# Performance work log

Hardware: AMD Instinct MI355X
Metric: run time of the kernel (lower is better)

The kernel has to match this reference:

```python
import jax, jax.numpy as jnp
import numpy as np

B, T, D = 64, 1024, 512
U = 512  # num_units == input dim (GRULayer default)


def setup_inputs() -> dict:
    key = jax.random.key(0)
    k1, k2, k3, k4 = jax.random.split(key, 4)
    scale_k = 1.0 / np.sqrt(D)
    scale_r = 1.0 / np.sqrt(U)
    x = jax.random.normal(k1, (B, T, D), dtype=jnp.float32)
    kernel = jax.random.normal(k2, (D, 3 * U), dtype=jnp.float32) * scale_k
    recurrent_kernel = jax.random.normal(k3, (U, 3 * U), dtype=jnp.float32) * scale_r
    # Keras GRUCell reset_after=True: bias shape (2, 3U): input bias + recurrent bias
    bias = jax.random.normal(k4, (2, 3 * U), dtype=jnp.float32) * 0.01
    return {"x": x, "kernel": kernel, "recurrent_kernel": recurrent_kernel, "bias": bias}


def reference(x, kernel, recurrent_kernel, bias):
    """Keras GRUCell (reset_after=True) recurrence via layers.RNN.

    Returns only the final hidden state [B, U] (return_sequences=False).
    """
    b_i = bias[0]  # input bias [3U]
    b_r = bias[1]  # recurrent bias [3U]

    def step(h, x_t):
        # x_t: [B, D], h: [B, U]
        xm = x_t @ kernel + b_i                # [B, 3U]
        hm = h @ recurrent_kernel + b_r        # [B, 3U]
        xz, xr, xh = jnp.split(xm, 3, axis=-1)
        hz, hr, hh = jnp.split(hm, 3, axis=-1)
        z = jax.nn.sigmoid(xz + hz)            # update gate
        r = jax.nn.sigmoid(xr + hr)            # reset gate
        h_cand = jnp.tanh(xh + r * hh)
        h_new = z * h + (1.0 - z) * h_cand
        return h_new, None

    h0 = jnp.zeros((x.shape[0], U), dtype=x.dtype)
    xs = jnp.swapaxes(x, 0, 1)  # [T, B, D] for scan over time
    h_final, _ = jax.lax.scan(step, h0, xs)
    return h_final  # [B, U]
```

## Files before the change

kernel.cpp:

```cpp
#include <hip/hip_runtime.h>
#include <hip/hip_bf16.h>


typedef __attribute__((ext_vector_type(8))) short short8;
typedef __attribute__((ext_vector_type(4))) float f32x4;
typedef __attribute__((ext_vector_type(4))) unsigned int u32x4;

__device__ __forceinline__ unsigned short f2bf(float f) {
  unsigned u = __float_as_uint(f);
  u += 0x7FFFu + ((u >> 16) & 1u);
  return (unsigned short)(u >> 16);
}
__device__ __forceinline__ float bf2f(unsigned short s) {
  return __uint_as_float(((unsigned)s) << 16);
}

__global__ void transpose_cast(const float* __restrict__ src,
                               unsigned short* __restrict__ dst,
                               int R, int C) {
  __shared__ float tile[32][33];
  int c0 = blockIdx.x * 32, r0 = blockIdx.y * 32;
  int tx = threadIdx.x, ty = threadIdx.y;
#pragma unroll
  for (int i = 0; i < 4; i++) {
    tile[ty + i * 8][tx] = src[(size_t)(r0 + ty + i * 8) * C + c0 + tx];
  }
  __syncthreads();
#pragma unroll
  for (int i = 0; i < 4; i++) {
    dst[(size_t)(c0 + ty + i * 8) * R + r0 + tx] = f2bf(tile[tx][ty + i * 8]);
  }
}

__global__ __launch_bounds__(256) void xm_gemm(const float* __restrict__ x,
                                               const unsigned short* __restrict__ Wt,
                                               const float* __restrict__ bias,
                                               unsigned short* __restrict__ XM) {
  __shared__ unsigned short As[128][72];
  __shared__ unsigned short Bs[128][72];
  const int tid = threadIdx.x;
  const int bm = blockIdx.x;
  const int bn = blockIdx.y;
  const int wave = tid >> 6, lane = tid & 63;
  const int moff = (wave & 1) * 64, noff = (wave >> 1) * 64;

  f32x4 acc[4][4];
#pragma unroll
  for (int mt = 0; mt < 4; mt++)
#pragma unroll
    for (int nt = 0; nt < 4; nt++) acc[mt][nt] = (f32x4){0.f, 0.f, 0.f, 0.f};

  const int r = tid >> 1;
  const int kb = (tid & 1) * 32;
  const int rg = bm * 128 + r;
  const int bb = rg & 63, tt = rg >> 6;

  for (int k0 = 0; k0 < 512; k0 += 64) {
    const f32x4* xp4 = (const f32x4*)(x + ((size_t)bb * 1024 + tt) * 512 + k0 + kb);
#pragma unroll
    for (int j = 0; j < 4; j++) {
      f32x4 lo = xp4[2 * j];
      f32x4 hi = xp4[2 * j + 1];
      union { unsigned short us[8]; short8 v; } u;
      u.us[0] = f2bf(lo[0]); u.us[1] = f2bf(lo[1]); u.us[2] = f2bf(lo[2]); u.us[3] = f2bf(lo[3]);
      u.us[4] = f2bf(hi[0]); u.us[5] = f2bf(hi[1]); u.us[6] = f2bf(hi[2]); u.us[7] = f2bf(hi[3]);
      *(short8*)&As[r][kb + j * 8] = u.v;
    }
    const short8* wp8 = (const short8*)(Wt + (size_t)(bn * 128 + r) * 512 + k0 + kb);
#pragma unroll
    for (int j = 0; j < 4; j++) *(short8*)&Bs[r][kb + j * 8] = wp8[j];
    __syncthreads();

#pragma unroll
    for (int kk = 0; kk < 2; kk++) {
      short8 a[4], b[4];
#pragma unroll
      for (int mt = 0; mt < 4; mt++)
        a[mt] = *(const short8*)&As[moff + mt * 16 + (lane & 15)][kk * 32 + (lane >> 4) * 8];
#pragma unroll
      for (int nt = 0; nt < 4; nt++)
        b[nt] = *(const short8*)&Bs[noff + nt * 16 + (lane & 15)][kk * 32 + (lane >> 4) * 8];
#pragma unroll
      for (int mt = 0; mt < 4; mt++)
#pragma unroll
        for (int nt = 0; nt < 4; nt++)
          acc[mt][nt] = __builtin_amdgcn_mfma_f32_16x16x32_bf16(a[mt], b[nt], acc[mt][nt], 0, 0, 0);
    }
    __syncthreads();
  }

#pragma unroll
  for (int nt = 0; nt < 4; nt++) {
    const int cg = bn * 128 + noff + nt * 16 + (lane & 15);
    const float bi = bias[cg];
#pragma unroll
    for (int mt = 0; mt < 4; mt++) {
      const int rg2 = bm * 128 + moff + mt * 16 + (lane >> 4) * 4;
#pragma unroll
      for (int i = 0; i < 4; i++)
        XM[(size_t)(rg2 + i) * 1536 + cg] = f2bf(acc[mt][nt][i] + bi);
    }
  }
}

__global__ __launch_bounds__(256, 1) void gru_rec(const unsigned short* __restrict__ Rt,
                                                  const unsigned short* __restrict__ XM,
                                                  const float* __restrict__ bias,
                                                  unsigned int* ring,
                                                  unsigned int* flags,
                                                  float* __restrict__ out) {
  const int tid = threadIdx.x;
  const int lane = tid & 63;
  const int w = tid >> 6;
  const int blk = blockIdx.x;
  const int gi = blk >> 3;
  const int j = blk & 7;
  const int u0 = j * 64 + w * 16;
  const int col = lane & 15;
  const int krow = lane >> 4;
  const int hrow = col & 7;

  unsigned int* ring_g = ring + (size_t)gi * 4096;
  unsigned long long* ring64_g = (unsigned long long*)ring_g;
  unsigned int* flg = flags + gi * 32;

  __shared__ alignas(16) unsigned short hlds[8][512];

  short8 Bf[3][16];
#pragma unroll
  for (int g3 = 0; g3 < 3; g3++)
#pragma unroll
    for (int ks = 0; ks < 16; ks++)
      Bf[g3][ks] = *(const short8*)(Rt + (size_t)(g3 * 512 + u0 + col) * 512 + ks * 32 + krow * 8);

  const float br0 = bias[1536 + 0 * 512 + u0 + col];
  const float br1 = bias[1536 + 1 * 512 + u0 + col];
  const float br2 = bias[1536 + 2 * 512 + u0 + col];

  float hreg[4] = {0.f, 0.f, 0.f, 0.f};

  const int g1 = tid, g2 = tid + 256;
  const int r1 = g1 >> 6, c1s = (g1 & 63) ^ r1;
  const int r2 = g2 >> 6, c2s = (g2 & 63) ^ r2;

  unsigned short xc[3][4], xn[3][4];
#pragma unroll
  for (int g3 = 0; g3 < 3; g3++)
#pragma unroll
    for (int i = 0; i < 4; i++) {
      int batch = gi * 8 + ((krow * 4 + i) & 7);
      xc[g3][i] = XM[(size_t)batch * 1536 + g3 * 512 + u0 + col];
    }

#pragma unroll 1
  for (int t = 0; t < 1024; ++t) {
    f32x4 acc0 = (f32x4){0.f, 0.f, 0.f, 0.f};
    f32x4 acc1 = acc0, acc2 = acc0;

    if (t > 0) {
      if (w == 0) {
        const unsigned tgt = (unsigned)t;
        for (;;) {
          unsigned v = (lane < 8)
              ? __hip_atomic_load(&flg[lane], __ATOMIC_RELAXED, __HIP_MEMORY_SCOPE_AGENT)
              : tgt;
          if (__all((int)(v >= tgt))) break;
          __builtin_amdgcn_s_sleep(1);
        }
      }
      __syncthreads();

      const unsigned long long* rp = ring64_g + (size_t)((t + 1) & 1) * 1024;
      unsigned long long qa0 = __hip_atomic_load(rp + 2 * g1, __ATOMIC_RELAXED,
                                                 __HIP_MEMORY_SCOPE_AGENT);
      unsigned long long qa1 = __hip_atomic_load(rp + 2 * g1 + 1, __ATOMIC_RELAXED,
                                                 __HIP_MEMORY_SCOPE_AGENT);
      unsigned long long qb0 = __hip_atomic_load(rp + 2 * g2, __ATOMIC_RELAXED,
                                                 __HIP_MEMORY_SCOPE_AGENT);
      unsigned long long qb1 = __hip_atomic_load(rp + 2 * g2 + 1, __ATOMIC_RELAXED,
                                                 __HIP_MEMORY_SCOPE_AGENT);

      *(u32x4*)&hlds[r1][c1s * 8] =
          (u32x4){(unsigned)qa0, (unsigned)(qa0 >> 32), (unsigned)qa1, (unsigned)(qa1 >> 32)};
      *(u32x4*)&hlds[r2][c2s * 8] =
          (u32x4){(unsigned)qb0, (unsigned)(qb0 >> 32), (unsigned)qb1, (unsigned)(qb1 >> 32)};
      __syncthreads();

      short8 Af[16];
#pragma unroll
      for (int ks = 0; ks < 16; ++ks)
        Af[ks] = *(const short8*)&hlds[hrow][(((ks << 2) + krow) ^ hrow) * 8];
#pragma unroll
      for (int ks = 0; ks < 16; ++ks) {
        acc0 = __builtin_amdgcn_mfma_f32_16x16x32_bf16(Af[ks], Bf[0][ks], acc0, 0, 0, 0);
        acc1 = __builtin_amdgcn_mfma_f32_16x16x32_bf16(Af[ks], Bf[1][ks], acc1, 0, 0, 0);
        acc2 = __builtin_amdgcn_mfma_f32_16x16x32_bf16(Af[ks], Bf[2][ks], acc2, 0, 0, 0);
      }
    }

#pragma unroll
    for (int i = 0; i < 4; i++) {
      float hz = acc0[i] + br0;
      float hr = acc1[i] + br1;
      float hh = acc2[i] + br2;
      float xz = bf2f(xc[0][i]);
      float xr = bf2f(xc[1][i]);
      float xh = bf2f(xc[2][i]);
      float z = 1.f / (1.f + __expf(-(xz + hz)));
      float r = 1.f / (1.f + __expf(-(xr + hr)));
      float y = xh + r * hh;
      float ay = fabsf(y);
      float e = __expf(-2.f * ay);
      float ca = (1.f - e) / (1.f + e);
      ca = (y < 0.f) ? -ca : ca;
      hreg[i] = z * hreg[i] + (1.f - z) * ca;
    }

    if (t < 1023) {
      unsigned int* hw = ring_g + (size_t)(t & 1) * 2048;
#pragma unroll
      for (int i = 0; i < 4; i++) {
        int lb = krow * 4 + i;
        float other = __shfl_xor(hreg[i], 1);
        if (krow < 2 && (col & 1) == 0) {
          unsigned d = (unsigned)f2bf(hreg[i]) | ((unsigned)f2bf(other) << 16);
          __hip_atomic_store(hw + (size_t)lb * 256 + ((u0 + col) >> 1), d,
                             __ATOMIC_RELAXED, __HIP_MEMORY_SCOPE_AGENT);
        }
      }
      asm volatile("s_waitcnt vmcnt(0)" ::: "memory");
      __syncthreads();
      if (tid == 0) {
        __hip_atomic_store(&flg[j], (unsigned)(t + 1),
                           __ATOMIC_RELAXED, __HIP_MEMORY_SCOPE_AGENT);
      }
    }

    const int tn = (t < 1023) ? t + 1 : 1023;
#pragma unroll
    for (int g3 = 0; g3 < 3; g3++)
#pragma unroll
      for (int i = 0; i < 4; i++) {
        int batch = gi * 8 + ((krow * 4 + i) & 7);
        xn[g3][i] = XM[(size_t)(tn * 64 + batch) * 1536 + g3 * 512 + u0 + col];
      }
#pragma unroll
    for (int g3 = 0; g3 < 3; g3++)
#pragma unroll
      for (int i = 0; i < 4; i++) xc[g3][i] = xn[g3][i];
  }

  if (krow < 2) {
#pragma unroll
    for (int i = 0; i < 4; i++)
      out[(size_t)(gi * 8 + krow * 4 + i) * 512 + u0 + col] = hreg[i];
  }
}

extern "C" void kernel_launch(void* const* d_in, const int* in_sizes, int n_in,
                              void* d_out, int out_size, void* d_ws, size_t ws_size,
                              hipStream_t stream) {
  const float* x = (const float*)d_in[0];
  const float* W = (const float*)d_in[1];
  const float* R = (const float*)d_in[2];
  const float* bias = (const float*)d_in[3];
  float* out = (float*)d_out;

  char* ws = (char*)d_ws;
  unsigned int* flags = (unsigned int*)(ws + 0);
  unsigned short* Wt = (unsigned short*)(ws + 135168);
  unsigned int* ring = (unsigned int*)(ws + 135168);
  unsigned short* Rt = (unsigned short*)(ws + 1708032);
  unsigned short* XM = (unsigned short*)(ws + 3280896);

  hipMemsetAsync(flags, 0, 4096, stream);
  transpose_cast<<<dim3(48, 16), dim3(32, 8), 0, stream>>>(W, Wt, 512, 1536);
  transpose_cast<<<dim3(48, 16), dim3(32, 8), 0, stream>>>(R, Rt, 512, 1536);
  xm_gemm<<<dim3(512, 12), dim3(256), 0, stream>>>(x, Wt, bias, XM);
  gru_rec<<<dim3(64), dim3(256), 0, stream>>>(Rt, XM, bias, ring, flags, out);
}
```

Before: 3.470 ms.

## Replace per-block flag handshake with tagged ring entries polled directly

```diff
diff --git a/kernel.cpp b/kernel.cpp
--- a/kernel.cpp
+++ b/kernel.cpp
@@ -106,8 +106,7 @@
 __global__ __launch_bounds__(256, 1) void gru_rec(const unsigned short* __restrict__ Rt,
                                                   const unsigned short* __restrict__ XM,
                                                   const float* __restrict__ bias,
-                                                  unsigned int* ring,
-                                                  unsigned int* flags,
+                                                  unsigned long long* ring,
                                                   float* __restrict__ out) {
   const int tid = threadIdx.x;
   const int lane = tid & 63;
@@ -120,9 +119,7 @@
   const int krow = lane >> 4;
   const int hrow = col & 7;
 
-  unsigned int* ring_g = ring + (size_t)gi * 4096;
-  unsigned long long* ring64_g = (unsigned long long*)ring_g;
-  unsigned int* flg = flags + gi * 32;
+  unsigned long long* ring_g = ring + (size_t)gi * 4096;
 
   __shared__ alignas(16) unsigned short hlds[8][512];
 
@@ -139,9 +136,9 @@
 
   float hreg[4] = {0.f, 0.f, 0.f, 0.f};
 
-  const int g1 = tid, g2 = tid + 256;
-  const int r1 = g1 >> 6, c1s = (g1 & 63) ^ r1;
-  const int r2 = g2 >> 6, c2s = (g2 & 63) ^ r2;
+  const int c1 = tid, c2 = tid + 256;
+  const int r1 = c1 >> 6, c1s = (c1 & 63) ^ r1;
+  const int r2 = c2 >> 6, c2s = (c2 & 63) ^ r2;
 
   unsigned short xc[3][4], xn[3][4];
 #pragma unroll
@@ -158,38 +155,35 @@
     f32x4 acc1 = acc0, acc2 = acc0;
 
     if (t > 0) {
-      if (w == 0) {
-        const unsigned tgt = (unsigned)t;
-        for (;;) {
-          unsigned v = (lane < 8)
-              ? __hip_atomic_load(&flg[lane], __ATOMIC_RELAXED, __HIP_MEMORY_SCOPE_AGENT)
-              : tgt;
-          if (__all((int)(v >= tgt))) break;
-          __builtin_amdgcn_s_sleep(1);
+      const unsigned tagv = (unsigned)t;
+      const unsigned long long* rp = ring_g + (size_t)((t + 1) & 1) * 2048;
+      unsigned long long q[8];
+      for (;;) {
+        unsigned bad = 0;
+#pragma unroll
+        for (int k = 0; k < 4; ++k) {
+          q[k] = __hip_atomic_load(rp + 4 * c1 + k, __ATOMIC_RELAXED,
+                                   __HIP_MEMORY_SCOPE_AGENT);
+          q[4 + k] = __hip_atomic_load(rp + 4 * c2 + k, __ATOMIC_RELAXED,
+                                       __HIP_MEMORY_SCOPE_AGENT);
         }
-      }
-      __syncthreads();
-
-      const unsigned long long* rp = ring64_g + (size_t)((t + 1) & 1) * 1024;
-      unsigned long long qa0 = __hip_atomic_load(rp + 2 * g1, __ATOMIC_RELAXED,
-                                                 __HIP_MEMORY_SCOPE_AGENT);
-      unsigned long long qa1 = __hip_atomic_load(rp + 2 * g1 + 1, __ATOMIC_RELAXED,
-                                                 __HIP_MEMORY_SCOPE_AGENT);
-      unsigned long long qb0 = __hip_atomic_load(rp + 2 * g2, __ATOMIC_RELAXED,
-                                                 __HIP_MEMORY_SCOPE_AGENT);
-      unsigned long long qb1 = __hip_atomic_load(rp + 2 * g2 + 1, __ATOMIC_RELAXED,
-                                                 __HIP_MEMORY_SCOPE_AGENT);
+#pragma unroll
+        for (int k = 0; k < 8; ++k) bad |= ((unsigned)(q[k] >> 32)) ^ tagv;
+        if (__all((int)(bad == 0))) break;
+        __builtin_amdgcn_s_sleep(1);
+      }
 
       *(u32x4*)&hlds[r1][c1s * 8] =
-          (u32x4){(unsigned)qa0, (unsigned)(qa0 >> 32), (unsigned)qa1, (unsigned)(qa1 >> 32)};
+          (u32x4){(unsigned)q[0], (unsigned)q[1], (unsigned)q[2], (unsigned)q[3]};
       *(u32x4*)&hlds[r2][c2s * 8] =
-          (u32x4){(unsigned)qb0, (unsigned)(qb0 >> 32), (unsigned)qb1, (unsigned)(qb1 >> 32)};
+          (u32x4){(unsigned)q[4], (unsigned)q[5], (unsigned)q[6], (unsigned)q[7]};
       __syncthreads();
 
       short8 Af[16];
 #pragma unroll
       for (int ks = 0; ks < 16; ++ks)
         Af[ks] = *(const short8*)&hlds[hrow][(((ks << 2) + krow) ^ hrow) * 8];
+      __syncthreads();
 #pragma unroll
       for (int ks = 0; ks < 16; ++ks) {
         acc0 = __builtin_amdgcn_mfma_f32_16x16x32_bf16(Af[ks], Bf[0][ks], acc0, 0, 0, 0);
@@ -217,22 +211,18 @@
     }
 
     if (t < 1023) {
-      unsigned int* hw = ring_g + (size_t)(t & 1) * 2048;
+      unsigned long long* hw = ring_g + (size_t)(t & 1) * 2048;
+      const unsigned long long tagbits = ((unsigned long long)(unsigned)(t + 1)) << 32;
 #pragma unroll
       for (int i = 0; i < 4; i++) {
         int lb = krow * 4 + i;
         float other = __shfl_xor(hreg[i], 1);
         if (krow < 2 && (col & 1) == 0) {
           unsigned d = (unsigned)f2bf(hreg[i]) | ((unsigned)f2bf(other) << 16);
-          __hip_atomic_store(hw + (size_t)lb * 256 + ((u0 + col) >> 1), d,
+          __hip_atomic_store(hw + (size_t)lb * 256 + ((u0 + col) >> 1),
+                             tagbits | (unsigned long long)d,
                              __ATOMIC_RELAXED, __HIP_MEMORY_SCOPE_AGENT);
         }
-      }
-      asm volatile("s_waitcnt vmcnt(0)" ::: "memory");
-      __syncthreads();
-      if (tid == 0) {
-        __hip_atomic_store(&flg[j], (unsigned)(t + 1),
-                           __ATOMIC_RELAXED, __HIP_MEMORY_SCOPE_AGENT);
       }
     }
 
@@ -267,15 +257,14 @@
   float* out = (float*)d_out;
 
   char* ws = (char*)d_ws;
-  unsigned int* flags = (unsigned int*)(ws + 0);
   unsigned short* Wt = (unsigned short*)(ws + 135168);
-  unsigned int* ring = (unsigned int*)(ws + 135168);
+  unsigned long long* ring = (unsigned long long*)(ws + 135168);
   unsigned short* Rt = (unsigned short*)(ws + 1708032);
   unsigned short* XM = (unsigned short*)(ws + 3280896);
 
-  hipMemsetAsync(flags, 0, 4096, stream);
   transpose_cast<<<dim3(48, 16), dim3(32, 8), 0, stream>>>(W, Wt, 512, 1536);
   transpose_cast<<<dim3(48, 16), dim3(32, 8), 0, stream>>>(R, Rt, 512, 1536);
   xm_gemm<<<dim3(512, 12), dim3(256), 0, stream>>>(x, Wt, bias, XM);
-  gru_rec<<<dim3(64), dim3(256), 0, stream>>>(Rt, XM, bias, ring, flags, out);
-}
+  hipMemsetAsync(ring, 0, 8ull * 2 * 8 * 256 * 8, stream);
+  gru_rec<<<dim3(64), dim3(256), 0, stream>>>(Rt, XM, bias, ring, out);
+}
```

New measurement: 3.019 ms. 1.15x faster.
